# Optimization experiments

Hardware: AMD Instinct MI355X
Metric: run time of the kernel (lower is better)

Reference implementation:

```python
import jax, jax.numpy as jnp
import numpy as np

D_MODEL = 1024
NUM_HEADS = 16
HEAD_DIM = D_MODEL // NUM_HEADS


def setup_inputs() -> dict:
    key = jax.random.key(0)
    ks = jax.random.split(key, 9)
    s = 1.0 / np.sqrt(D_MODEL)
    x = jax.random.normal(ks[0], (2, 2048, D_MODEL), dtype=jnp.float32)
    Wq = jax.random.normal(ks[1], (D_MODEL, D_MODEL), dtype=jnp.float32) * s
    bq = jnp.zeros((D_MODEL,), dtype=jnp.float32)
    Wk = jax.random.normal(ks[2], (D_MODEL, D_MODEL), dtype=jnp.float32) * s
    bk = jnp.zeros((D_MODEL,), dtype=jnp.float32)
    Wv = jax.random.normal(ks[3], (D_MODEL, D_MODEL), dtype=jnp.float32) * s
    bv = jnp.zeros((D_MODEL,), dtype=jnp.float32)
    Wo = jax.random.normal(ks[4], (D_MODEL, D_MODEL), dtype=jnp.float32) * s
    bo = jnp.zeros((D_MODEL,), dtype=jnp.float32)
    return {"x": x, "Wq": Wq, "bq": bq, "Wk": Wk, "bk": bk,
            "Wv": Wv, "bv": bv, "Wo": Wo, "bo": bo}


def reference(x, Wq, bq, Wk, bk, Wv, bv, Wo, bo):
    B, S, D = x.shape
    H, Hd = NUM_HEADS, HEAD_DIM
    scale = 1.0 / np.sqrt(Hd)

    def split_heads(t):  # [B,S,D] -> [B,H,S,Hd]
        return t.reshape(B, S, H, Hd).transpose(0, 2, 1, 3)

    q = split_heads(x @ Wq + bq)
    k = split_heads(x @ Wk + bk)
    v = split_heads(x @ Wv + bv)

    scores = jnp.einsum('bhqd,bhkd->bhqk', q, k) * scale
    scores = scores - jnp.max(scores, axis=-1, keepdims=True)
    attn = jax.nn.softmax(scores, axis=-1)
    attended = jnp.einsum('bhqk,bhkd->bhqd', attn, v)
    attended = attended.transpose(0, 2, 1, 3).reshape(B, S, D)
    return attended @ Wo + bo
```

## Files before the change

kernel.cpp:

```cpp
#include <hip/hip_runtime.h>
#include <hip/hip_bf16.h>

typedef __bf16 bf16_t;
typedef __bf16 bf16x8 __attribute__((ext_vector_type(8)));
typedef __bf16 bf16x4 __attribute__((ext_vector_type(4)));
typedef float floatx4 __attribute__((ext_vector_type(4)));
typedef short short4v __attribute__((ext_vector_type(4)));

#define D_MODEL 1024
#define SEQ     2048
#define BATCH   2
#define NHEAD   16
#define HDIM    64
#define MTOT    (BATCH * SEQ)
#define LROWS   (32 * 2048)

#define QSCALE  0.18033688011112042f

union PBu { bf16x4 b; short4v s; };

__device__ __forceinline__ void async_copy16(const bf16_t* g, bf16_t* l) {
    __builtin_amdgcn_global_load_lds(
        (const __attribute__((address_space(1))) void*)g,
        (__attribute__((address_space(3))) void*)l, 16, 0, 0);
}

__global__ void prep_kernel(
    const float* __restrict__ x, bf16_t* __restrict__ xb,
    const float* __restrict__ W0, const float* __restrict__ W1,
    const float* __restrict__ W2, const float* __restrict__ W3,
    bf16_t* __restrict__ T0, bf16_t* __restrict__ T1,
    bf16_t* __restrict__ T2, bf16_t* __restrict__ T3)
{
    const int z = blockIdx.z;
    const int tx = threadIdx.x, ty = threadIdx.y;
    if (z == 4) {
        const int lin = (blockIdx.y * 32 + blockIdx.x) * 256 + ty * 32 + tx;
        const int base = lin * 16;
#pragma unroll
        for (int c = 0; c < 4; ++c) {
            const float4 v = *(const float4*)(x + base + c * 4);
            bf16x4 o = { (bf16_t)v.x, (bf16_t)v.y, (bf16_t)v.z, (bf16_t)v.w };
            *(bf16x4*)(xb + base + c * 4) = o;
        }
        return;
    }
    __shared__ float tile[32][33];
    const float* W = (z == 0) ? W0 : (z == 1) ? W1 : (z == 2) ? W2 : W3;
    bf16_t*     Wt = (z == 0) ? T0 : (z == 1) ? T1 : (z == 2) ? T2 : T3;
    const int k0 = blockIdx.y * 32, n0 = blockIdx.x * 32;
#pragma unroll
    for (int j = 0; j < 32; j += 8)
        tile[ty + j][tx] = W[(size_t)(k0 + ty + j) * D_MODEL + n0 + tx];
    __syncthreads();
#pragma unroll
    for (int j = 0; j < 32; j += 8)
        Wt[(size_t)(n0 + ty + j) * D_MODEL + k0 + tx] = (bf16_t)tile[tx][ty + j];
}

__device__ __forceinline__ void gemm_mainloop(
    const bf16_t* __restrict__ A, const bf16_t* __restrict__ Bt,
    int m0, int n0, bf16_t* As, bf16_t* Bs, floatx4 acc[4][4])
{
    const int tid  = threadIdx.x;
    const int lane = tid & 63;
    const int wid  = tid >> 6;
    const int quad = lane >> 4;
    const int col  = lane & 15;
    const int wm   = (wid >> 1) * 64;
    const int wn   = (wid & 1) * 64;
    const int srow = tid >> 3;
    const int scc  = ((tid & 7) ^ (srow & 7)) * 8;
    const int xorc = col & 7;

    const bf16_t* Ag = A  + (size_t)(m0 + srow) * D_MODEL + scc;
    const bf16_t* Bg = Bt + (size_t)(n0 + srow) * D_MODEL + scc;
    bf16_t* Al = As + tid * 8;
    bf16_t* Bl = Bs + tid * 8;

    for (int kb = 0; kb < D_MODEL; kb += 64) {
#pragma unroll
        for (int p = 0; p < 4; ++p) {
            async_copy16(Ag + kb + p * (32 * D_MODEL), Al + p * 2048);
            async_copy16(Bg + kb + p * (32 * D_MODEL), Bl + p * 2048);
        }
        __syncthreads();
#pragma unroll
        for (int kh = 0; kh < 2; ++kh) {
            bf16x8 af[4], bfr[4];
#pragma unroll
            for (int i = 0; i < 4; ++i)
                af[i] = *(const bf16x8*)(As + (wm + i * 16 + col) * 64 + (((kh * 4 + quad) ^ xorc) * 8));
#pragma unroll
            for (int j = 0; j < 4; ++j)
                bfr[j] = *(const bf16x8*)(Bs + (wn + j * 16 + col) * 64 + (((kh * 4 + quad) ^ xorc) * 8));
#pragma unroll
            for (int i = 0; i < 4; ++i)
#pragma unroll
                for (int j = 0; j < 4; ++j)
                    acc[i][j] = __builtin_amdgcn_mfma_f32_16x16x32_bf16(af[i], bfr[j], acc[i][j], 0, 0, 0);
        }
        __syncthreads();
    }
}

__global__ __launch_bounds__(256, 3) void gemm_qkv(
    const bf16_t* __restrict__ xb,
    const bf16_t* __restrict__ Wtq, const bf16_t* __restrict__ Wtk, const bf16_t* __restrict__ Wtv,
    const float* __restrict__ bq, const float* __restrict__ bk, const float* __restrict__ bv,
    bf16_t* __restrict__ Q, bf16_t* __restrict__ Kh, bf16_t* __restrict__ Vt)
{
    __shared__ bf16_t As[128 * 64];
    __shared__ bf16_t Bs[128 * 64];
    const int z = blockIdx.z;
    const bf16_t* Bt   = (z == 0) ? Wtq : (z == 1) ? Wtk : Wtv;
    const float*  bias = (z == 0) ? bq  : (z == 1) ? bk  : bv;
    bf16_t*       O    = (z == 0) ? Q   : (z == 1) ? Kh  : Vt;
    const float   qs   = (z == 0) ? QSCALE : 1.0f;
    const int m0 = blockIdx.y * 128;
    const int n0 = blockIdx.x * 128;

    floatx4 acc[4][4];
#pragma unroll
    for (int i = 0; i < 4; ++i)
#pragma unroll
        for (int j = 0; j < 4; ++j)
            acc[i][j] = (floatx4){0.f, 0.f, 0.f, 0.f};

    gemm_mainloop(xb, Bt, m0, n0, As, Bs, acc);

    const int tid  = threadIdx.x;
    const int lane = tid & 63;
    const int wid  = tid >> 6;
    const int quad = lane >> 4;
    const int col  = lane & 15;
    const int wm   = (wid >> 1) * 64;
    const int wn   = (wid & 1) * 64;

    if (z == 2) {
#pragma unroll
        for (int i = 0; i < 4; ++i) {
#pragma unroll
            for (int j = 0; j < 4; ++j) {
                const int n = n0 + wn + j * 16 + col;
                const float bb = bias[n];
                const int mb = m0 + wm + i * 16 + quad * 4;
                const size_t bhb = (size_t)((mb >> 11) * NHEAD + (n >> 6)) * (SEQ * HDIM);
                bf16x4 pk = { (bf16_t)(acc[i][j][0] + bb), (bf16_t)(acc[i][j][1] + bb),
                              (bf16_t)(acc[i][j][2] + bb), (bf16_t)(acc[i][j][3] + bb) };
                *(bf16x4*)(O + bhb + (size_t)(n & 63) * SEQ + (mb & 2047)) = pk;
            }
        }
    } else {
#pragma unroll
        for (int i = 0; i < 4; ++i) {
#pragma unroll
            for (int j = 0; j < 4; ++j) {
                const int n = n0 + wn + j * 16 + col;
                const float bb = bias[n];
#pragma unroll
                for (int r = 0; r < 4; ++r) {
                    const int m = m0 + wm + i * 16 + quad * 4 + r;
                    const float v = (acc[i][j][r] + bb) * qs;
                    const size_t bhb = (size_t)((m >> 11) * NHEAD + (n >> 6)) * (SEQ * HDIM);
                    O[bhb + (size_t)(m & 2047) * HDIM + (n & 63)] = (bf16_t)v;
                }
            }
        }
    }
}

__global__ __launch_bounds__(128, 4) void attn_kernel(
    const bf16_t* __restrict__ Q, const bf16_t* __restrict__ K,
    const bf16_t* __restrict__ Vt, bf16_t* __restrict__ Opart, float* __restrict__ lpart)
{
    __shared__ bf16_t Ks[64 * 64];
    __shared__ bf16_t Vs[64 * 64];

    const int tid  = threadIdx.x;
    const int lane = tid & 63;
    const int wid  = tid >> 6;
    const int quad = lane >> 4;
    const int col  = lane & 15;
    const int xorc = col & 7;

    const int blk = blockIdx.x;
    const int idx = blk >> 3;
    const int bh  = (blk & 7) * 4 + (idx >> 6);
    const int rem = idx & 63;
    const int sp  = rem >> 5;
    const int q0  = (rem & 31) * 64;

    const bf16_t* Qb = Q  + (size_t)bh * (SEQ * HDIM);
    const bf16_t* Kb = K  + (size_t)bh * (SEQ * HDIM);
    const bf16_t* Vb = Vt + (size_t)bh * (SEQ * HDIM);

    bf16x8 qf[2][2];
#pragma unroll
    for (int st = 0; st < 2; ++st) {
        const int qrow = q0 + wid * 32 + st * 16 + col;
        qf[st][0] = *(const bf16x8*)(Qb + (size_t)qrow * HDIM + quad * 8);
        qf[st][1] = *(const bf16x8*)(Qb + (size_t)qrow * HDIM + 32 + quad * 8);
    }

    floatx4 o_acc[2][4];
    floatx4 l_acc[2];
#pragma unroll
    for (int st = 0; st < 2; ++st) {
        l_acc[st] = (floatx4){0.f, 0.f, 0.f, 0.f};
#pragma unroll
        for (int dt = 0; dt < 4; ++dt)
            o_acc[st][dt] = (floatx4){0.f, 0.f, 0.f, 0.f};
    }
    const short4v ones = { (short)0x3F80, (short)0x3F80, (short)0x3F80, (short)0x3F80 };

    const int srow = tid >> 3;
    const int scc  = ((tid & 7) ^ (srow & 7)) * 8;
    const bf16_t* Kg = Kb + (size_t)(sp * 1024 + srow) * HDIM + scc;
    const bf16_t* Vg = Vb + (size_t)srow * SEQ + sp * 1024 + scc;
    bf16_t* KsL = Ks + tid * 8;
    bf16_t* VsL = Vs + tid * 8;

    for (int it = 0; it < 16; ++it) {
        const int ko = it * 64;
#pragma unroll
        for (int p = 0; p < 4; ++p) {
            async_copy16(Kg + (size_t)(ko + p * 16) * HDIM, KsL + p * 1024);
            async_copy16(Vg + (size_t)(p * 16) * SEQ + ko, VsL + p * 1024);
        }
        __syncthreads();

        bf16x8 kf[4][2];
#pragma unroll
        for (int t = 0; t < 4; ++t) {
            kf[t][0] = *(const bf16x8*)(Ks + (t * 16 + col) * 64 + ((quad ^ xorc) * 8));
            kf[t][1] = *(const bf16x8*)(Ks + (t * 16 + col) * 64 + (((4 + quad) ^ xorc) * 8));
        }
        short4v vfr[4][4];
#pragma unroll
        for (int dt = 0; dt < 4; ++dt)
#pragma unroll
            for (int t = 0; t < 4; ++t) {
                const int sch = t * 2 + (quad >> 1);
                vfr[dt][t] = *(const short4v*)(Vs + (dt * 16 + col) * 64 + ((sch ^ xorc) * 8) + (quad & 1) * 4);
            }

#pragma unroll
        for (int st = 0; st < 2; ++st) {
            floatx4 s_acc[4];
            short4v pb[4];
#pragma unroll
            for (int t = 0; t < 4; ++t) {
                s_acc[t] = (floatx4){0.f, 0.f, 0.f, 0.f};
                s_acc[t] = __builtin_amdgcn_mfma_f32_16x16x32_bf16(kf[t][0], qf[st][0], s_acc[t], 0, 0, 0);
                s_acc[t] = __builtin_amdgcn_mfma_f32_16x16x32_bf16(kf[t][1], qf[st][1], s_acc[t], 0, 0, 0);
            }
#pragma unroll
            for (int t = 0; t < 4; ++t) {
                const float p0 = __builtin_amdgcn_exp2f(s_acc[t][0]);
                const float p1 = __builtin_amdgcn_exp2f(s_acc[t][1]);
                const float p2 = __builtin_amdgcn_exp2f(s_acc[t][2]);
                const float p3 = __builtin_amdgcn_exp2f(s_acc[t][3]);
                PBu u;
                u.b = (bf16x4){ (bf16_t)p0, (bf16_t)p1, (bf16_t)p2, (bf16_t)p3 };
                pb[t] = u.s;
                l_acc[st] = __builtin_amdgcn_mfma_f32_16x16x16bf16_1k(ones, pb[t], l_acc[st], 0, 0, 0);
            }
#pragma unroll
            for (int dt = 0; dt < 4; ++dt)
#pragma unroll
                for (int t = 0; t < 4; ++t)
                    o_acc[st][dt] = __builtin_amdgcn_mfma_f32_16x16x16bf16_1k(vfr[dt][t], pb[t], o_acc[st][dt], 0, 0, 0);
        }
        __syncthreads();
    }

#pragma unroll
    for (int st = 0; st < 2; ++st) {
        const float lsum = l_acc[st][0];
        const float inv  = 1.0f / lsum;
        const int qrow = q0 + wid * 32 + st * 16 + col;
        bf16_t* od = Opart + ((size_t)(sp * 32 + bh) * SEQ + qrow) * HDIM + quad * 4;
#pragma unroll
        for (int dt = 0; dt < 4; ++dt) {
            bf16x4 pk = { (bf16_t)(o_acc[st][dt][0] * inv), (bf16_t)(o_acc[st][dt][1] * inv),
                          (bf16_t)(o_acc[st][dt][2] * inv), (bf16_t)(o_acc[st][dt][3] * inv) };
            *(bf16x4*)(od + dt * 16) = pk;
        }
        if (quad == 0)
            lpart[(size_t)sp * LROWS + (size_t)bh * SEQ + qrow] = lsum;
    }
}

__global__ __launch_bounds__(256) void attn_combine(
    const bf16_t* __restrict__ Op, const float* __restrict__ lp, bf16_t* __restrict__ A2)
{
    const int tid = threadIdx.x;
    const int bh  = blockIdx.y;
    const int q   = blockIdx.x * 64 + (tid >> 2);
    const int dc  = (tid & 3) * 16;
    const int b   = bh >> 4, h = bh & 15;

    const float l0 = lp[(size_t)bh * SEQ + q];
    const float l1 = lp[LROWS + (size_t)bh * SEQ + q];
    const float rs = 1.0f / (l0 + l1);
    const float w0 = l0 * rs, w1 = l1 * rs;

    const size_t b0 = ((size_t)bh * SEQ + q) * HDIM + dc;
    const size_t b1 = ((size_t)(32 + bh) * SEQ + q) * HDIM + dc;
    bf16_t* dst = A2 + ((size_t)(b * SEQ + q)) * D_MODEL + h * HDIM + dc;
#pragma unroll
    for (int c = 0; c < 2; ++c) {
        const bf16x8 a = *(const bf16x8*)(Op + b0 + c * 8);
        const bf16x8 d = *(const bf16x8*)(Op + b1 + c * 8);
        bf16x8 o;
#pragma unroll
        for (int j = 0; j < 8; ++j)
            o[j] = (bf16_t)(w0 * (float)a[j] + w1 * (float)d[j]);
        *(bf16x8*)(dst + c * 8) = o;
    }
}

__global__ __launch_bounds__(256, 3) void gemm_proj(
    const bf16_t* __restrict__ A2, const bf16_t* __restrict__ Wto,
    const float* __restrict__ bo, float* __restrict__ out)
{
    __shared__ bf16_t As[64 * 64];
    __shared__ bf16_t Bs[128 * 64];
    const int m0 = blockIdx.y * 64;
    const int n0 = blockIdx.x * 128;

    const int tid  = threadIdx.x;
    const int lane = tid & 63;
    const int wid  = tid >> 6;
    const int quad = lane >> 4;
    const int col  = lane & 15;
    const int wm   = (wid >> 1) * 32;
    const int wn   = (wid & 1) * 64;
    const int srow = tid >> 3;
    const int scc  = ((tid & 7) ^ (srow & 7)) * 8;
    const int xorc = col & 7;

    floatx4 acc[2][4];
#pragma unroll
    for (int i = 0; i < 2; ++i)
#pragma unroll
        for (int j = 0; j < 4; ++j)
            acc[i][j] = (floatx4){0.f, 0.f, 0.f, 0.f};

    const bf16_t* Ag = A2  + (size_t)(m0 + srow) * D_MODEL + scc;
    const bf16_t* Bg = Wto + (size_t)(n0 + srow) * D_MODEL + scc;
    bf16_t* Al = As + tid * 8;
    bf16_t* Bl = Bs + tid * 8;

    for (int kb = 0; kb < D_MODEL; kb += 64) {
#pragma unroll
        for (int p = 0; p < 2; ++p)
            async_copy16(Ag + kb + p * (32 * D_MODEL), Al + p * 2048);
#pragma unroll
        for (int p = 0; p < 4; ++p)
            async_copy16(Bg + kb + p * (32 * D_MODEL), Bl + p * 2048);
        __syncthreads();
#pragma unroll
        for (int kh = 0; kh < 2; ++kh) {
            bf16x8 af[2], bfr[4];
#pragma unroll
            for (int i = 0; i < 2; ++i)
                af[i] = *(const bf16x8*)(As + (wm + i * 16 + col) * 64 + (((kh * 4 + quad) ^ xorc) * 8));
#pragma unroll
            for (int j = 0; j < 4; ++j)
                bfr[j] = *(const bf16x8*)(Bs + (wn + j * 16 + col) * 64 + (((kh * 4 + quad) ^ xorc) * 8));
#pragma unroll
            for (int i = 0; i < 2; ++i)
#pragma unroll
                for (int j = 0; j < 4; ++j)
                    acc[i][j] = __builtin_amdgcn_mfma_f32_16x16x32_bf16(af[i], bfr[j], acc[i][j], 0, 0, 0);
        }
        __syncthreads();
    }

#pragma unroll
    for (int i = 0; i < 2; ++i) {
#pragma unroll
        for (int j = 0; j < 4; ++j) {
            const int n = n0 + wn + j * 16 + col;
            const float bb = bo[n];
#pragma unroll
            for (int r = 0; r < 4; ++r) {
                const int m = m0 + wm + i * 16 + quad * 4 + r;
                out[(size_t)m * D_MODEL + n] = acc[i][j][r] + bb;
            }
        }
    }
}

extern "C" void kernel_launch(void* const* d_in, const int* in_sizes, int n_in,
                              void* d_out, int out_size, void* d_ws, size_t ws_size,
                              hipStream_t stream) {
    const float* x  = (const float*)d_in[0];
    const float* Wq = (const float*)d_in[1];
    const float* bq = (const float*)d_in[2];
    const float* Wk = (const float*)d_in[3];
    const float* bk = (const float*)d_in[4];
    const float* Wv = (const float*)d_in[5];
    const float* bv = (const float*)d_in[6];
    const float* Wo = (const float*)d_in[7];
    const float* bo = (const float*)d_in[8];
    float* out = (float*)d_out;

    const size_t MB = 1ull << 20;
    char* ws = (char*)d_ws;
    bf16_t* Q     = (bf16_t*)(ws + 0 * MB);
    bf16_t* Kh    = (bf16_t*)(ws + 8 * MB);
    bf16_t* Vt    = (bf16_t*)(ws + 16 * MB);
    bf16_t* A2    = (bf16_t*)(ws + 24 * MB);
    bf16_t* xb    = (bf16_t*)(ws + 32 * MB);
    float*  lpart = (float*)(ws + 32 * MB);
    bf16_t* Wtq   = (bf16_t*)(ws + 40 * MB);
    bf16_t* Wtk   = (bf16_t*)(ws + 42 * MB);
    bf16_t* Wtv   = (bf16_t*)(ws + 44 * MB);
    bf16_t* Wto   = (bf16_t*)(ws + 46 * MB);
    bf16_t* Opart = (bf16_t*)(ws + 48 * MB);

    prep_kernel<<<dim3(32, 32, 5), dim3(32, 8), 0, stream>>>(
        x, xb, Wq, Wk, Wv, Wo, Wtq, Wtk, Wtv, Wto);

    gemm_qkv<<<dim3(D_MODEL / 128, MTOT / 128, 3), 256, 0, stream>>>(
        xb, Wtq, Wtk, Wtv, bq, bk, bv, Q, Kh, Vt);

    attn_kernel<<<dim3(2048), 128, 0, stream>>>(Q, Kh, Vt, Opart, lpart);

    attn_combine<<<dim3(SEQ / 64, BATCH * NHEAD), 256, 0, stream>>>(Opart, lpart, A2);

    gemm_proj<<<dim3(D_MODEL / 128, MTOT / 64), 256, 0, stream>>>(A2, Wto, bo, out);
}
```

Baseline: 191.8 us.

## Fuse split-softmax combine into projection GEMM and stage QKV epilogue via LDS

Removes the separate attn_combine kernel by having gemm_proj read both partial attention outputs and their row sums directly and blend them while filling the A tile in shared memory. This drops the A2 round trip through global memory, but replaces async global-to-LDS copies with synchronous loads and arithmetic inside the GEMM main loop, and each N-block repeats the blend work. The QKV GEMM epilogue now stages results in padded shared memory so it can issue coalesced 16-byte stores instead of scattered 2-byte ones. The prep kernel also switches to 64x32 tiles with vectorized loads and 16-byte bf16 stores for the weight transpose.

```diff
diff --git a/kernel.cpp b/kernel.cpp
--- a/kernel.cpp
+++ b/kernel.cpp
@@ -14,6 +14,7 @@
 #define HDIM    64
 #define MTOT    (BATCH * SEQ)
 #define LROWS   (32 * 2048)
+#define OSPLIT  ((size_t)LROWS * HDIM)
 
 #define QSCALE  0.18033688011112042f
 
@@ -33,29 +34,40 @@
     bf16_t* __restrict__ T2, bf16_t* __restrict__ T3)
 {
     const int z = blockIdx.z;
-    const int tx = threadIdx.x, ty = threadIdx.y;
+    const int tid = threadIdx.x;
     if (z == 4) {
-        const int lin = (blockIdx.y * 32 + blockIdx.x) * 256 + ty * 32 + tx;
-        const int base = lin * 16;
-#pragma unroll
-        for (int c = 0; c < 4; ++c) {
+        const int lin = blockIdx.y * 32 + blockIdx.x;
+        const int base = (lin * 256 + tid) * 32;
+#pragma unroll
+        for (int c = 0; c < 8; ++c) {
             const float4 v = *(const float4*)(x + base + c * 4);
             bf16x4 o = { (bf16_t)v.x, (bf16_t)v.y, (bf16_t)v.z, (bf16_t)v.w };
             *(bf16x4*)(xb + base + c * 4) = o;
         }
         return;
     }
-    __shared__ float tile[32][33];
+    __shared__ float tf[64][37];
     const float* W = (z == 0) ? W0 : (z == 1) ? W1 : (z == 2) ? W2 : W3;
     bf16_t*     Wt = (z == 0) ? T0 : (z == 1) ? T1 : (z == 2) ? T2 : T3;
-    const int k0 = blockIdx.y * 32, n0 = blockIdx.x * 32;
-#pragma unroll
-    for (int j = 0; j < 32; j += 8)
-        tile[ty + j][tx] = W[(size_t)(k0 + ty + j) * D_MODEL + n0 + tx];
+    const int n0 = blockIdx.x * 32, k0 = blockIdx.y * 64;
+    const int kr = tid >> 3;
+    const int nc = (tid & 7) * 4;
+#pragma unroll
+    for (int p = 0; p < 2; ++p) {
+        const float4 v = *(const float4*)(W + (size_t)(k0 + kr + p * 32) * D_MODEL + n0 + nc);
+        tf[kr + p * 32][nc + 0] = v.x;
+        tf[kr + p * 32][nc + 1] = v.y;
+        tf[kr + p * 32][nc + 2] = v.z;
+        tf[kr + p * 32][nc + 3] = v.w;
+    }
     __syncthreads();
-#pragma unroll
-    for (int j = 0; j < 32; j += 8)
-        Wt[(size_t)(n0 + ty + j) * D_MODEL + k0 + tx] = (bf16_t)tile[tx][ty + j];
+    const int nr = tid >> 3;
+    const int kc = (tid & 7) * 8;
+    bf16x8 o;
+#pragma unroll
+    for (int j = 0; j < 8; ++j)
+        o[j] = (bf16_t)tf[kc + j][nr];
+    *(bf16x8*)(Wt + (size_t)(n0 + nr) * D_MODEL + k0 + kc) = o;
 }
 
 __device__ __forceinline__ void gemm_mainloop(
@@ -110,8 +122,10 @@
     const float* __restrict__ bq, const float* __restrict__ bk, const float* __restrict__ bv,
     bf16_t* __restrict__ Q, bf16_t* __restrict__ Kh, bf16_t* __restrict__ Vt)
 {
-    __shared__ bf16_t As[128 * 64];
-    __shared__ bf16_t Bs[128 * 64];
+    __shared__ bf16_t smem[128 * 136];
+    bf16_t* As = smem;
+    bf16_t* Bs = smem + 8192;
+
     const int z = blockIdx.z;
     const bf16_t* Bt   = (z == 0) ? Wtq : (z == 1) ? Wtk : Wtv;
     const float*  bias = (z == 0) ? bq  : (z == 1) ? bk  : bv;
@@ -142,13 +156,11 @@
         for (int i = 0; i < 4; ++i) {
 #pragma unroll
             for (int j = 0; j < 4; ++j) {
-                const int n = n0 + wn + j * 16 + col;
-                const float bb = bias[n];
-                const int mb = m0 + wm + i * 16 + quad * 4;
-                const size_t bhb = (size_t)((mb >> 11) * NHEAD + (n >> 6)) * (SEQ * HDIM);
+                const int n_l = wn + j * 16 + col;
+                const float bb = bias[n0 + n_l];
                 bf16x4 pk = { (bf16_t)(acc[i][j][0] + bb), (bf16_t)(acc[i][j][1] + bb),
                               (bf16_t)(acc[i][j][2] + bb), (bf16_t)(acc[i][j][3] + bb) };
-                *(bf16x4*)(O + bhb + (size_t)(n & 63) * SEQ + (mb & 2047)) = pk;
+                *(bf16x4*)(smem + n_l * 136 + wm + i * 16 + quad * 4) = pk;
             }
         }
     } else {
@@ -156,16 +168,37 @@
         for (int i = 0; i < 4; ++i) {
 #pragma unroll
             for (int j = 0; j < 4; ++j) {
-                const int n = n0 + wn + j * 16 + col;
-                const float bb = bias[n];
+                const int n_l = wn + j * 16 + col;
+                const float bb = bias[n0 + n_l];
 #pragma unroll
                 for (int r = 0; r < 4; ++r) {
-                    const int m = m0 + wm + i * 16 + quad * 4 + r;
-                    const float v = (acc[i][j][r] + bb) * qs;
-                    const size_t bhb = (size_t)((m >> 11) * NHEAD + (n >> 6)) * (SEQ * HDIM);
-                    O[bhb + (size_t)(m & 2047) * HDIM + (n & 63)] = (bf16_t)v;
+                    const int m_l = wm + i * 16 + quad * 4 + r;
+                    smem[m_l * 136 + n_l] = (bf16_t)((acc[i][j][r] + bb) * qs);
                 }
             }
+        }
+    }
+    __syncthreads();
+
+    if (z == 2) {
+#pragma unroll
+        for (int c = 0; c < 8; ++c) {
+            const int row = wid * 32 + c * 4 + quad;
+            const bf16x8 v = *(const bf16x8*)(smem + row * 136 + col * 8);
+            const int n_g = n0 + row;
+            const size_t base = (size_t)((m0 >> 11) * NHEAD + (n_g >> 6)) * (SEQ * HDIM)
+                              + (size_t)(n_g & 63) * SEQ + (m0 & 2047) + col * 8;
+            *(bf16x8*)(O + base) = v;
+        }
+    } else {
+#pragma unroll
+        for (int c = 0; c < 8; ++c) {
+            const int row = wid * 32 + c * 4 + quad;
+            const bf16x8 v = *(const bf16x8*)(smem + row * 136 + col * 8);
+            const int n_g = n0 + col * 8;
+            const size_t base = (size_t)((m0 >> 11) * NHEAD + (n_g >> 6)) * (SEQ * HDIM)
+                              + (size_t)((m0 & 2047) + row) * HDIM + (n_g & 63);
+            *(bf16x8*)(O + base) = v;
         }
     }
 }
@@ -292,38 +325,10 @@
     }
 }
 
-__global__ __launch_bounds__(256) void attn_combine(
-    const bf16_t* __restrict__ Op, const float* __restrict__ lp, bf16_t* __restrict__ A2)
-{
-    const int tid = threadIdx.x;
-    const int bh  = blockIdx.y;
-    const int q   = blockIdx.x * 64 + (tid >> 2);
-    const int dc  = (tid & 3) * 16;
-    const int b   = bh >> 4, h = bh & 15;
-
-    const float l0 = lp[(size_t)bh * SEQ + q];
-    const float l1 = lp[LROWS + (size_t)bh * SEQ + q];
-    const float rs = 1.0f / (l0 + l1);
-    const float w0 = l0 * rs, w1 = l1 * rs;
-
-    const size_t b0 = ((size_t)bh * SEQ + q) * HDIM + dc;
-    const size_t b1 = ((size_t)(32 + bh) * SEQ + q) * HDIM + dc;
-    bf16_t* dst = A2 + ((size_t)(b * SEQ + q)) * D_MODEL + h * HDIM + dc;
-#pragma unroll
-    for (int c = 0; c < 2; ++c) {
-        const bf16x8 a = *(const bf16x8*)(Op + b0 + c * 8);
-        const bf16x8 d = *(const bf16x8*)(Op + b1 + c * 8);
-        bf16x8 o;
-#pragma unroll
-        for (int j = 0; j < 8; ++j)
-            o[j] = (bf16_t)(w0 * (float)a[j] + w1 * (float)d[j]);
-        *(bf16x8*)(dst + c * 8) = o;
-    }
-}
-
 __global__ __launch_bounds__(256, 3) void gemm_proj(
-    const bf16_t* __restrict__ A2, const bf16_t* __restrict__ Wto,
-    const float* __restrict__ bo, float* __restrict__ out)
+    const bf16_t* __restrict__ Op, const float* __restrict__ lp,
+    const bf16_t* __restrict__ Wto, const float* __restrict__ bo,
+    float* __restrict__ out)
 {
     __shared__ bf16_t As[64 * 64];
     __shared__ bf16_t Bs[128 * 64];
@@ -348,15 +353,29 @@
         for (int j = 0; j < 4; ++j)
             acc[i][j] = (floatx4){0.f, 0.f, 0.f, 0.f};
 
-    const bf16_t* Ag = A2  + (size_t)(m0 + srow) * D_MODEL + scc;
+    const int b  = m0 >> 11;
+    const int qA = (m0 & 2047) + srow;
     const bf16_t* Bg = Wto + (size_t)(n0 + srow) * D_MODEL + scc;
-    bf16_t* Al = As + tid * 8;
     bf16_t* Bl = Bs + tid * 8;
 
     for (int kb = 0; kb < D_MODEL; kb += 64) {
-#pragma unroll
-        for (int p = 0; p < 2; ++p)
-            async_copy16(Ag + kb + p * (32 * D_MODEL), Al + p * 2048);
+        const int bhq = (b * NHEAD + (kb >> 6)) * SEQ;
+#pragma unroll
+        for (int p = 0; p < 2; ++p) {
+            const int q = qA + p * 32;
+            const float l0 = lp[bhq + q];
+            const float l1 = lp[LROWS + bhq + q];
+            const float rs = 1.0f / (l0 + l1);
+            const float w0 = l0 * rs, w1 = l1 * rs;
+            const size_t o0 = (size_t)(bhq + q) * HDIM + scc;
+            const bf16x8 a0 = *(const bf16x8*)(Op + o0);
+            const bf16x8 a1 = *(const bf16x8*)(Op + OSPLIT + o0);
+            bf16x8 oo;
+#pragma unroll
+            for (int j2 = 0; j2 < 8; ++j2)
+                oo[j2] = (bf16_t)(w0 * (float)a0[j2] + w1 * (float)a1[j2]);
+            *(bf16x8*)(As + p * 2048 + tid * 8) = oo;
+        }
 #pragma unroll
         for (int p = 0; p < 4; ++p)
             async_copy16(Bg + kb + p * (32 * D_MODEL), Bl + p * 2048);
@@ -413,8 +432,7 @@
     bf16_t* Q     = (bf16_t*)(ws + 0 * MB);
     bf16_t* Kh    = (bf16_t*)(ws + 8 * MB);
     bf16_t* Vt    = (bf16_t*)(ws + 16 * MB);
-    bf16_t* A2    = (bf16_t*)(ws + 24 * MB);
-    bf16_t* xb    = (bf16_t*)(ws + 32 * MB);
+    bf16_t* xb    = (bf16_t*)(ws + 24 * MB);
     float*  lpart = (float*)(ws + 32 * MB);
     bf16_t* Wtq   = (bf16_t*)(ws + 40 * MB);
     bf16_t* Wtk   = (bf16_t*)(ws + 42 * MB);
@@ -422,7 +440,7 @@
     bf16_t* Wto   = (bf16_t*)(ws + 46 * MB);
     bf16_t* Opart = (bf16_t*)(ws + 48 * MB);
 
-    prep_kernel<<<dim3(32, 32, 5), dim3(32, 8), 0, stream>>>(
+    prep_kernel<<<dim3(32, 16, 5), 256, 0, stream>>>(
         x, xb, Wq, Wk, Wv, Wo, Wtq, Wtk, Wtv, Wto);
 
     gemm_qkv<<<dim3(D_MODEL / 128, MTOT / 128, 3), 256, 0, stream>>>(
@@ -430,7 +448,6 @@
 
     attn_kernel<<<dim3(2048), 128, 0, stream>>>(Q, Kh, Vt, Opart, lpart);
 
-    attn_combine<<<dim3(SEQ / 64, BATCH * NHEAD), 256, 0, stream>>>(Opart, lpart, A2);
-
-    gemm_proj<<<dim3(D_MODEL / 128, MTOT / 64), 256, 0, stream>>>(A2, Wto, bo, out);
-}
+    gemm_proj<<<dim3(D_MODEL / 128, MTOT / 64), 256, 0, stream>>>(
+        Opart, lpart, Wto, bo, out);
+}
```

After: 211.0 us. 10.0% more time.
